# Optimization experiments

Measured on AMD Instinct MI355X. Metric: run time of the kernel, lower is better.

The kernel has to match this reference:

```python
import jax, jax.numpy as jnp
import numpy as np

D = 1024      # model dim
H = 16        # heads
DH = 64       # dim per head (lucidrains default)
DEPTH = 6
MLP = 2048
P = 32
PD = 3 * P * P   # 3072
NC = 1000
B = 4         # packed sequences
N = 640       # tokens per packed sequence (incl. padding)
M = 18        # images per packed sequence
GRID = 8      # image_size // patch_size
SIZES = [(8,8),(8,8),(7,7),(7,7),(6,8),(8,6),(6,6),(5,7),(7,5),(5,5),(4,8),(8,4),(4,6),(6,4),(4,4),(3,5),(5,3),(3,3)]
SCALE = DH ** -0.5


def _pack_meta():
    hs, ws, ids = [], [], []
    for i, (h, w) in enumerate(SIZES):
        hh, ww = np.meshgrid(np.arange(h), np.arange(w), indexing='ij')
        hs.append(hh.ravel()); ws.append(ww.ravel()); ids.append(np.full(h * w, i))
    h = np.concatenate(hs); w = np.concatenate(ws); ii = np.concatenate(ids)
    pad = N - h.shape[0]
    h = np.pad(h, (0, pad)); w = np.pad(w, (0, pad))
    ii = np.pad(ii, (0, pad), constant_values=-1)  # padding tokens form their own block
    return (np.tile(h, (B, 1)).astype(np.int32),
            np.tile(w, (B, 1)).astype(np.int32),
            np.tile(ii, (B, 1)).astype(np.int32))


def _ln(x, g, b, eps=1e-5):
    m = x.mean(-1, keepdims=True)
    v = ((x - m) ** 2).mean(-1, keepdims=True)
    return (x - m) * jax.lax.rsqrt(v + eps) * g + b


def _heads(t):  # [b, n, H*DH] -> [b, H, n, DH]
    return t.reshape(t.shape[0], t.shape[1], H, DH).swapaxes(1, 2)


def _mha(q_in, kv_in, mask, Wq, Wkv, Wo, qn_g, qn_b, kn_g, kn_b):
    # NaViT attention: pre-norm applied by caller to q_in; per-head qk LayerNorm; no biases.
    q = _ln(_heads(q_in @ Wq), qn_g, qn_b)
    k, v = jnp.split(kv_in @ Wkv, 2, axis=-1)
    k = _ln(_heads(k), kn_g, kn_b)
    v = _heads(v)
    dots = jnp.einsum('bhid,bhjd->bhij', q, k) * SCALE
    dots = jnp.where(mask, dots, jnp.finfo(dots.dtype).min)
    o = jnp.einsum('bhij,bhjd->bhid', jax.nn.softmax(dots, axis=-1), v)
    o = o.swapaxes(1, 2).reshape(o.shape[0], -1, H * DH)
    return o @ Wo


def _forward(patches, pe_ln1_g, pe_ln1_b, W_pe, b_pe, pe_ln2_g, pe_ln2_b, pos_h, pos_w,
             ln1_g, ln1_b, qn_g, qn_b, kn_g, kn_b, Wq, Wkv, Wo, ln2_g, ln2_b,
             W1, b1, W2, b2, fin_g, fin_b, pool_q, pl_ln_g, pl_ln_b, pl_qn_g, pl_qn_b,
             pl_kn_g, pl_kn_b, pl_Wq, pl_Wkv, pl_Wo, head_g, head_b, W_head, b_head,
             h_idx, w_idx, image_ids):
    # patch embedding: LN -> Linear -> LN, then factorized 2D pos embed
    x = _ln(patches, pe_ln1_g, pe_ln1_b) @ W_pe + b_pe
    x = _ln(x, pe_ln2_g, pe_ln2_b)
    x = x + pos_h[h_idx] + pos_w[w_idx]
    # block-diagonal attention mask: tokens attend only within their own image
    blk = (image_ids[:, :, None] == image_ids[:, None, :])[:, None]  # [B,1,N,N]
    for l in range(DEPTH):
        xn = _ln(x, ln1_g[l], ln1_b[l])
        x = x + _mha(xn, xn, blk, Wq[l], Wkv[l], Wo[l], qn_g[l], qn_b[l], kn_g[l], kn_b[l])
        xn = _ln(x, ln2_g[l], ln2_b[l])
        x = x + jax.nn.gelu(xn @ W1[l] + b1[l], approximate=False) @ W2[l] + b2[l]
    x = _ln(x, fin_g, fin_b)
    # attention pooling: one learned query per packed image (context NOT re-normed, as in na_vit)
    queries = jnp.broadcast_to(pool_q, (B, M, D))
    qn = _ln(queries, pl_ln_g, pl_ln_b)
    pmask = (jnp.arange(M)[None, :, None] == image_ids[:, None, :])[:, None]  # [B,1,M,N]
    pooled = _mha(qn, x, pmask, pl_Wq, pl_Wkv, pl_Wo, pl_qn_g, pl_qn_b, pl_kn_g, pl_kn_b) + queries
    pooled = pooled.reshape(B * M, D)
    return _ln(pooled, head_g, head_b) @ W_head + b_head  # [B*M, 1000]


def setup_inputs() -> dict:
    key = jax.random.key(0)
    ks = iter(jax.random.split(key, 32))
    h_idx, w_idx, image_ids = _pack_meta()
    f32 = jnp.float32
    d = dict(
        patches=jax.random.normal(next(ks), (B, N, PD), f32),
        pe_ln1_g=jnp.ones((PD,), f32), pe_ln1_b=jnp.zeros((PD,), f32),
        W_pe=0.02 * jax.random.normal(next(ks), (PD, D), f32), b_pe=jnp.zeros((D,), f32),
        pe_ln2_g=jnp.ones((D,), f32), pe_ln2_b=jnp.zeros((D,), f32),
        pos_h=0.02 * jax.random.normal(next(ks), (GRID, D), f32),
        pos_w=0.02 * jax.random.normal(next(ks), (GRID, D), f32),
        ln1_g=jnp.ones((DEPTH, D), f32), ln1_b=jnp.zeros((DEPTH, D), f32),
        qn_g=jnp.ones((DEPTH, DH), f32), qn_b=jnp.zeros((DEPTH, DH), f32),
        kn_g=jnp.ones((DEPTH, DH), f32), kn_b=jnp.zeros((DEPTH, DH), f32),
        Wq=0.02 * jax.random.normal(next(ks), (DEPTH, D, H * DH), f32),
        Wkv=0.02 * jax.random.normal(next(ks), (DEPTH, D, 2 * H * DH), f32),
        Wo=0.02 * jax.random.normal(next(ks), (DEPTH, H * DH, D), f32),
        ln2_g=jnp.ones((DEPTH, D), f32), ln2_b=jnp.zeros((DEPTH, D), f32),
        W1=0.02 * jax.random.normal(next(ks), (DEPTH, D, MLP), f32), b1=jnp.zeros((DEPTH, MLP), f32),
        W2=0.02 * jax.random.normal(next(ks), (DEPTH, MLP, D), f32), b2=jnp.zeros((DEPTH, D), f32),
        fin_g=jnp.ones((D,), f32), fin_b=jnp.zeros((D,), f32),
        pool_q=0.02 * jax.random.normal(next(ks), (D,), f32),
        pl_ln_g=jnp.ones((D,), f32), pl_ln_b=jnp.zeros((D,), f32),
        pl_qn_g=jnp.ones((DH,), f32), pl_qn_b=jnp.zeros((DH,), f32),
        pl_kn_g=jnp.ones((DH,), f32), pl_kn_b=jnp.zeros((DH,), f32),
        pl_Wq=0.02 * jax.random.normal(next(ks), (D, H * DH), f32),
        pl_Wkv=0.02 * jax.random.normal(next(ks), (D, 2 * H * DH), f32),
        pl_Wo=0.02 * jax.random.normal(next(ks), (H * DH, D), f32),
        head_g=jnp.ones((D,), f32), head_b=jnp.zeros((D,), f32),
        W_head=0.02 * jax.random.normal(next(ks), (D, NC), f32), b_head=jnp.zeros((NC,), f32),
        h_idx=jnp.asarray(h_idx), w_idx=jnp.asarray(w_idx), image_ids=jnp.asarray(image_ids),
    )
    return d


def reference(patches, pe_ln1_g, pe_ln1_b, W_pe, b_pe, pe_ln2_g, pe_ln2_b, pos_h, pos_w,
              ln1_g, ln1_b, qn_g, qn_b, kn_g, kn_b, Wq, Wkv, Wo, ln2_g, ln2_b,
              W1, b1, W2, b2, fin_g, fin_b, pool_q, pl_ln_g, pl_ln_b, pl_qn_g, pl_qn_b,
              pl_kn_g, pl_kn_b, pl_Wq, pl_Wkv, pl_Wo, head_g, head_b, W_head, b_head,
              h_idx, w_idx, image_ids):
    return _forward(patches, pe_ln1_g, pe_ln1_b, W_pe, b_pe, pe_ln2_g, pe_ln2_b, pos_h, pos_w,
                    ln1_g, ln1_b, qn_g, qn_b, kn_g, kn_b, Wq, Wkv, Wo, ln2_g, ln2_b,
                    W1, b1, W2, b2, fin_g, fin_b, pool_q, pl_ln_g, pl_ln_b, pl_qn_g, pl_qn_b,
                    pl_kn_g, pl_kn_b, pl_Wq, pl_Wkv, pl_Wo, head_g, head_b, W_head, b_head,
                    h_idx, w_idx, image_ids)
```

## Files before the change

kernel.cpp:

```cpp
#include <hip/hip_runtime.h>
#include <cmath>

constexpr int kB = 4, kN = 640, kD = 1024, kH = 16, kDH = 64;
constexpr int kDepth = 6, kMLP = 2048, kPD = 3072, kNC = 1000, kM = 18;
constexpr float kScale = 0.125f;
constexpr float kNegInf = -3.4028235e38f;

typedef __bf16 bf16;
typedef __attribute__((ext_vector_type(8))) __bf16 bf16x8;
typedef __attribute__((ext_vector_type(4))) __bf16 bf16x4;
typedef __attribute__((ext_vector_type(4))) float f32x4;

#define AS1 __attribute__((address_space(1)))
#define AS3 __attribute__((address_space(3)))

__device__ __forceinline__ void gload16(const void* g, void* l) {
  __builtin_amdgcn_global_load_lds((AS1 void*)g, (AS3 void*)l, 16, 0, 0);
}

constexpr size_t kMEG = 1048576;
constexpr size_t kOffPe = 0;
constexpr size_t kLayer0 = 3 * kMEG;
constexpr size_t kLayerSz = 8 * kMEG;
constexpr size_t kOffPool = kLayer0 + 6 * kLayerSz;
constexpr size_t kOffPlWq = kOffPool;
constexpr size_t kOffPlWkv = kOffPool + 1 * kMEG;
constexpr size_t kOffPlWo = kOffPool + 3 * kMEG;
constexpr size_t kOffHead = kOffPool + 4 * kMEG;
constexpr size_t kWtTotal = kOffHead + 1 * kMEG;

__global__ __launch_bounds__(256) void wt_all_kernel(
    const float* __restrict__ pe, const float* __restrict__ wq,
    const float* __restrict__ wkv, const float* __restrict__ wo,
    const float* __restrict__ w1, const float* __restrict__ w2,
    const float* __restrict__ plq, const float* __restrict__ plkv,
    const float* __restrict__ plo, const float* __restrict__ whead,
    bf16* __restrict__ WTB) {
  const int j = blockIdx.y;
  const float* W;
  size_t doff;
  int K, Nc, Np;
  if (j == 0) {
    W = pe; K = 3072; Nc = 1024; Np = 1024; doff = kOffPe;
  } else if (j < 31) {
    const int l = (j - 1) / 5, w = (j - 1) % 5;
    const size_t lbase = kLayer0 + (size_t)l * kLayerSz;
    switch (w) {
      case 0:  W = wq  + (size_t)l * kMEG;     K = 1024; Nc = 1024; doff = lbase;            break;
      case 1:  W = wkv + (size_t)l * 2 * kMEG; K = 1024; Nc = 2048; doff = lbase + kMEG;     break;
      case 2:  W = wo  + (size_t)l * kMEG;     K = 1024; Nc = 1024; doff = lbase + 3 * kMEG; break;
      case 3:  W = w1  + (size_t)l * 2 * kMEG; K = 1024; Nc = 2048; doff = lbase + 4 * kMEG; break;
      default: W = w2  + (size_t)l * 2 * kMEG; K = 2048; Nc = 1024; doff = lbase + 6 * kMEG; break;
    }
    Np = Nc;
  } else if (j == 31) { W = plq;  K = 1024; Nc = 1024; Np = 1024; doff = kOffPlWq; }
  else if (j == 32)   { W = plkv; K = 1024; Nc = 2048; Np = 2048; doff = kOffPlWkv; }
  else if (j == 33)   { W = plo;  K = 1024; Nc = 1024; Np = 1024; doff = kOffPlWo; }
  else                { W = whead; K = 1024; Nc = 1000; Np = 1024; doff = kOffHead; }
  const int nbx = Np >> 5;
  const int ntiles = nbx * (K >> 5);
  const int tile = blockIdx.x;
  if (tile >= ntiles) return;
  const int n0 = (tile % nbx) * 32, k0 = (tile / nbx) * 32;
  bf16* WT = WTB + doff;
  __shared__ float s[32][33];
  const int tx = threadIdx.x & 31, ty = threadIdx.x >> 5;
#pragma unroll
  for (int i = 0; i < 4; ++i) {
    const int k = ty + i * 8;
    s[k][tx] = (n0 + tx < Nc) ? W[(size_t)(k0 + k) * Nc + (n0 + tx)] : 0.f;
  }
  __syncthreads();
#pragma unroll
  for (int i = 0; i < 4; ++i) {
    const int n = ty + i * 8;
    WT[(size_t)(n0 + n) * K + (k0 + tx)] = (bf16)s[tx][n];
  }
}

template <typename OT>
__global__ __launch_bounds__(256) void ln_kernel(
    const float* __restrict__ in, OT* __restrict__ out,
    const float* __restrict__ g, const float* __restrict__ b, int K) {
  const int row = blockIdx.x;
  const float* x = in + (size_t)row * K;
  OT* o = out + (size_t)row * K;
  const int K4 = K >> 2;
  float s = 0.f, s2 = 0.f;
  for (int c = threadIdx.x; c < K4; c += 256) {
    const float4 v = ((const float4*)x)[c];
    s += v.x + v.y + v.z + v.w;
    s2 += v.x * v.x + v.y * v.y + v.z * v.z + v.w * v.w;
  }
#pragma unroll
  for (int off = 32; off; off >>= 1) { s += __shfl_down(s, off); s2 += __shfl_down(s2, off); }
  __shared__ float ls[4], ls2[4];
  __shared__ float sm, sr;
  const int wid = threadIdx.x >> 6, lane = threadIdx.x & 63;
  if (lane == 0) { ls[wid] = s; ls2[wid] = s2; }
  __syncthreads();
  if (threadIdx.x == 0) {
    float a = ls[0] + ls[1] + ls[2] + ls[3];
    float a2 = ls2[0] + ls2[1] + ls2[2] + ls2[3];
    float mean = a / K;
    float var = a2 / K - mean * mean;
    sm = mean; sr = rsqrtf(var + 1e-5f);
  }
  __syncthreads();
  const float mean = sm, r = sr;
  for (int c = threadIdx.x; c < K4; c += 256) {
    const float4 v = ((const float4*)x)[c];
    const float4 gv = ((const float4*)g)[c];
    const float4 bv = ((const float4*)b)[c];
    const int d = c * 4;
    o[d + 0] = (OT)((v.x - mean) * r * gv.x + bv.x);
    o[d + 1] = (OT)((v.y - mean) * r * gv.y + bv.y);
    o[d + 2] = (OT)((v.z - mean) * r * gv.z + bv.z);
    o[d + 3] = (OT)((v.w - mean) * r * gv.w + bv.w);
  }
}

__global__ __launch_bounds__(256) void ln_pos_kernel(
    const float* __restrict__ in, float* __restrict__ out,
    const float* __restrict__ g, const float* __restrict__ b,
    const float* __restrict__ ph, const float* __restrict__ pw,
    const int* __restrict__ hi, const int* __restrict__ wi) {
  const int row = blockIdx.x;
  const float* x = in + (size_t)row * kD;
  float* o = out + (size_t)row * kD;
  float s = 0.f, s2 = 0.f;
  for (int c = threadIdx.x; c < 256; c += 256) {
    const float4 v = ((const float4*)x)[c];
    s += v.x + v.y + v.z + v.w;
    s2 += v.x * v.x + v.y * v.y + v.z * v.z + v.w * v.w;
  }
#pragma unroll
  for (int off = 32; off; off >>= 1) { s += __shfl_down(s, off); s2 += __shfl_down(s2, off); }
  __shared__ float ls[4], ls2[4];
  __shared__ float sm, sr;
  const int wid = threadIdx.x >> 6, lane = threadIdx.x & 63;
  if (lane == 0) { ls[wid] = s; ls2[wid] = s2; }
  __syncthreads();
  if (threadIdx.x == 0) {
    float a = ls[0] + ls[1] + ls[2] + ls[3];
    float a2 = ls2[0] + ls2[1] + ls2[2] + ls2[3];
    float mean = a / kD;
    float var = a2 / kD - mean * mean;
    sm = mean; sr = rsqrtf(var + 1e-5f);
  }
  __syncthreads();
  const float mean = sm, r = sr;
  const float4* phr = (const float4*)(ph + (size_t)hi[row] * kD);
  const float4* pwr = (const float4*)(pw + (size_t)wi[row] * kD);
  const int c = threadIdx.x;
  const float4 v = ((const float4*)x)[c];
  const float4 gv = ((const float4*)g)[c];
  const float4 bv = ((const float4*)b)[c];
  const float4 hv = phr[c], wv = pwr[c];
  float4 ov;
  ov.x = (v.x - mean) * r * gv.x + bv.x + hv.x + wv.x;
  ov.y = (v.y - mean) * r * gv.y + bv.y + hv.y + wv.y;
  ov.z = (v.z - mean) * r * gv.z + bv.z + hv.z + wv.z;
  ov.w = (v.w - mean) * r * gv.w + bv.w + hv.w + wv.w;
  ((float4*)o)[c] = ov;
}

__global__ __launch_bounds__(64) void headln_kernel(
    float* __restrict__ p, int stride,
    const float* __restrict__ g, const float* __restrict__ b) {
  const int blk = blockIdx.x;
  const int outer = blk / kH, h = blk % kH;
  float* x = p + (size_t)outer * stride + h * kDH;
  const int lane = threadIdx.x;
  float v = x[lane];
  float s = v, s2 = v * v;
#pragma unroll
  for (int off = 32; off; off >>= 1) { s += __shfl_xor(s, off); s2 += __shfl_xor(s2, off); }
  const float m = s * (1.f / kDH);
  const float var = s2 * (1.f / kDH) - m * m;
  const float r = rsqrtf(var + 1e-5f);
  x[lane] = (v - m) * r * g[lane] + b[lane];
}

__global__ __launch_bounds__(256) void poolq_kernel(
    const float* __restrict__ pq, const float* __restrict__ lg,
    const float* __restrict__ lb, const bf16* __restrict__ WqT,
    const float* __restrict__ qg, const float* __restrict__ qb,
    float* __restrict__ qpool) {
  const int h = blockIdx.x, tid = threadIdx.x;
  __shared__ float qs[1024];
  __shared__ float red[256];
  __shared__ float ls[4], ls2[4];
  __shared__ float sm, sr;
  const float4 v = ((const float4*)pq)[tid];
  float s = v.x + v.y + v.z + v.w;
  float s2 = v.x * v.x + v.y * v.y + v.z * v.z + v.w * v.w;
#pragma unroll
  for (int off = 32; off; off >>= 1) { s += __shfl_down(s, off); s2 += __shfl_down(s2, off); }
  const int wid = tid >> 6, lane = tid & 63;
  if (lane == 0) { ls[wid] = s; ls2[wid] = s2; }
  __syncthreads();
  if (tid == 0) {
    float a = ls[0] + ls[1] + ls[2] + ls[3];
    float a2 = ls2[0] + ls2[1] + ls2[2] + ls2[3];
    float mean = a / kD;
    sm = mean; sr = rsqrtf(a2 / kD - mean * mean + 1e-5f);
  }
  __syncthreads();
  {
    const float mean = sm, r = sr;
    const float4 gv = ((const float4*)lg)[tid];
    const float4 bv = ((const float4*)lb)[tid];
    qs[tid * 4 + 0] = (v.x - mean) * r * gv.x + bv.x;
    qs[tid * 4 + 1] = (v.y - mean) * r * gv.y + bv.y;
    qs[tid * 4 + 2] = (v.z - mean) * r * gv.z + bv.z;
    qs[tid * 4 + 3] = (v.w - mean) * r * gv.w + bv.w;
  }
  __syncthreads();
  const int d = tid & 63, qq = tid >> 6;
  const bf16* wrow = WqT + (size_t)(h * 64 + d) * 1024 + qq * 256;
  const float* qp = qs + qq * 256;
  float part = 0.f;
  for (int k = 0; k < 256; k += 8) {
    const bf16x8 w8 = *(const bf16x8*)(wrow + k);
#pragma unroll
    for (int e = 0; e < 8; ++e) part += qp[k + e] * (float)w8[e];
  }
  red[tid] = part;
  __syncthreads();
  if (tid < 64) {
    const float dot = red[tid] + red[tid + 64] + red[tid + 128] + red[tid + 192];
    float hs = dot, hs2 = dot * dot;
#pragma unroll
    for (int off = 32; off; off >>= 1) { hs += __shfl_xor(hs, off); hs2 += __shfl_xor(hs2, off); }
    const float m = hs * (1.f / kDH);
    const float r = rsqrtf(hs2 * (1.f / kDH) - m * m + 1e-5f);
    qpool[h * 64 + tid] = (dot - m) * r * qg[tid] + qb[tid];
  }
}

template <int NI, bool OUT_BF, bool GELU>
__global__ __launch_bounds__(256) void gemm64_kernel(
    const bf16* __restrict__ A, const bf16* __restrict__ WT,
    float* __restrict__ Cf, bf16* __restrict__ Cb,
    const float* __restrict__ bias, const float* __restrict__ res,
    int K, int Ncol, int nbx) {
  constexpr int BN = NI * 32;
  __shared__ __align__(16) bf16 As[2][64 * 64];
  __shared__ __align__(16) bf16 Bs[2][BN * 64];
  const int tid = threadIdx.x, lane = tid & 63, wid = tid >> 6;
  const int wr = wid >> 1, wc = wid & 1;
  const int cpx = gridDim.x >> 3;
  const int swz = (blockIdx.x & 7) * cpx + (blockIdx.x >> 3);
  const int row0 = (swz / nbx) * 64, col0 = (swz % nbx) * BN;
  const int fr = lane & 15, fg = lane >> 4;
  f32x4 acc[2][NI] = {};
  bf16* sA = As[0]; bf16* sB = Bs[0];
  bf16* dA = As[1]; bf16* dB = Bs[1];

  auto stage = [&](bf16* tA, bf16* tB, int kt) {
#pragma unroll
    for (int i = 0; i < 2; ++i) {
      const int c = i * 256 + tid;
      const int r = c >> 3, ci = c & 7;
      gload16(A + (size_t)(row0 + r) * K + kt + ((ci ^ (r & 7)) * 8),
              tA + (i * 256 + wid * 64) * 8);
    }
#pragma unroll
    for (int i = 0; i < NI; ++i) {
      const int c = i * 256 + tid;
      const int r = c >> 3, ci = c & 7;
      gload16(WT + (size_t)(col0 + r) * K + kt + ((ci ^ (r & 7)) * 8),
              tB + (i * 256 + wid * 64) * 8);
    }
  };
  auto compute = [&](const bf16* tA, const bf16* tB) {
#pragma unroll
    for (int kk = 0; kk < 2; ++kk) {
      bf16x8 af[2], bfr[NI];
#pragma unroll
      for (int mi = 0; mi < 2; ++mi) {
        const int r = wr * 32 + mi * 16 + fr;
        af[mi] = *(const bf16x8*)(tA + r * 64 + (((kk * 4 + fg) ^ (r & 7)) * 8));
      }
#pragma unroll
      for (int ni = 0; ni < NI; ++ni) {
        const int r = wc * (NI * 16) + ni * 16 + fr;
        bfr[ni] = *(const bf16x8*)(tB + r * 64 + (((kk * 4 + fg) ^ (r & 7)) * 8));
      }
#pragma unroll
      for (int mi = 0; mi < 2; ++mi)
#pragma unroll
        for (int ni = 0; ni < NI; ++ni)
          acc[mi][ni] = __builtin_amdgcn_mfma_f32_16x16x32_bf16(af[mi], bfr[ni], acc[mi][ni], 0, 0, 0);
    }
  };

  const int NT = K >> 6;
  stage(sA, sB, 0);
  __syncthreads();
  for (int t = 1; t < NT; ++t) {
    stage(dA, dB, t * 64);
    compute(sA, sB);
    __syncthreads();
    bf16* u;
    u = sA; sA = dA; dA = u;
    u = sB; sB = dB; dB = u;
  }
  compute(sA, sB);

  const int rb = row0 + wr * 32 + fg * 4;
  const int cb = col0 + wc * (NI * 16) + fr;
#pragma unroll
  for (int mi = 0; mi < 2; ++mi) {
#pragma unroll
    for (int ni = 0; ni < NI; ++ni) {
      const int cc = cb + ni * 16;
      const float bb = bias ? bias[cc] : 0.f;
#pragma unroll
      for (int r = 0; r < 4; ++r) {
        const int rr = rb + mi * 16 + r;
        float v = acc[mi][ni][r] + bb;
        if (res) v += res[(size_t)rr * Ncol + cc];
        if (GELU) v = 0.5f * v * (1.f + erff(v * 0.70710678118654752f));
        if (OUT_BF) Cb[(size_t)rr * Ncol + cc] = (bf16)v;
        else        Cf[(size_t)rr * Ncol + cc] = v;
      }
    }
  }
}

template <bool OUT_BF>
__global__ __launch_bounds__(256) void gemm_tail_kernel(
    const bf16* __restrict__ A, const bf16* __restrict__ WT,
    float* __restrict__ Cf, bf16* __restrict__ Cb,
    const float* __restrict__ bias, const float* __restrict__ resv,
    int Mr, int K, int Nc, int ldc, int resmode) {
  __shared__ __align__(16) bf16 As[64][40];
  __shared__ __align__(16) bf16 Bs[128][40];
  const int tid = threadIdx.x;
  const int lane = tid & 63, wid = tid >> 6;
  const int row0 = blockIdx.y * 64, col0 = blockIdx.x * 128;
  f32x4 acc[4][2] = {};
  const int am = tid >> 2, ako = (tid & 3) * 8;
  const int fr = lane & 15, fg = (lane >> 4) * 8;
  for (int k0 = 0; k0 < K; k0 += 32) {
    if (row0 + am < Mr)
      *(bf16x8*)&As[am][ako] = *(const bf16x8*)(A + (size_t)(row0 + am) * K + k0 + ako);
    else {
      bf16x8 z = {};
      *(bf16x8*)&As[am][ako] = z;
    }
#pragma unroll
    for (int it = 0; it < 2; ++it) {
      const int c = it * 256 + tid;
      const int n = c >> 2, ko = (c & 3) * 8;
      *(bf16x8*)&Bs[n][ko] = *(const bf16x8*)(WT + (size_t)(col0 + n) * K + k0 + ko);
    }
    __syncthreads();
    bf16x8 af[4], bfr[2];
#pragma unroll
    for (int mi = 0; mi < 4; ++mi) af[mi] = *(const bf16x8*)&As[mi * 16 + fr][fg];
#pragma unroll
    for (int ni = 0; ni < 2; ++ni) bfr[ni] = *(const bf16x8*)&Bs[wid * 32 + ni * 16 + fr][fg];
#pragma unroll
    for (int mi = 0; mi < 4; ++mi)
#pragma unroll
      for (int ni = 0; ni < 2; ++ni)
        acc[mi][ni] = __builtin_amdgcn_mfma_f32_16x16x32_bf16(af[mi], bfr[ni], acc[mi][ni], 0, 0, 0);
    __syncthreads();
  }
  const int r4 = (lane >> 4) * 4;
  const int cc0 = col0 + wid * 32 + (lane & 15);
#pragma unroll
  for (int mi = 0; mi < 4; ++mi) {
#pragma unroll
    for (int ni = 0; ni < 2; ++ni) {
      const int cc = cc0 + ni * 16;
      if (cc >= Nc) continue;
#pragma unroll
      for (int r = 0; r < 4; ++r) {
        const int rr = row0 + mi * 16 + r4 + r;
        if (rr >= Mr) continue;
        float v = acc[mi][ni][r];
        if (bias) v += bias[cc];
        if (resmode == 1) v += resv[(size_t)rr * ldc + cc];
        else if (resmode == 2) v += resv[cc];
        if (OUT_BF) Cb[(size_t)rr * ldc + cc] = (bf16)v;
        else        Cf[(size_t)rr * ldc + cc] = v;
      }
    }
  }
}

__global__ __launch_bounds__(256) void attn_kernel(
    const bf16* __restrict__ qkv, const int* __restrict__ ids,
    const float* __restrict__ qg, const float* __restrict__ qb,
    const float* __restrict__ kg, const float* __restrict__ kb,
    bf16* __restrict__ o) {
  const int h = blockIdx.x, img = blockIdx.y, b = blockIdx.z;
  const int tid = threadIdx.x, lane = tid & 63, wid = tid >> 6;
  __shared__ __align__(16) bf16 Qs[64][72];
  __shared__ __align__(16) bf16 Ks[64][72];
  __shared__ __align__(16) bf16 Vt[64][72];
  __shared__ __align__(16) bf16 Ps[64][72];
  __shared__ int wlo[4], whi[4];
  __shared__ int sLo, sHi;
  {
    const int want = (img < kM) ? img : -1;
    int lo = kN, hi = -1;
    for (int j = tid; j < kN; j += 256) {
      if (ids[b * kN + j] == want) { lo = min(lo, j); hi = max(hi, j); }
    }
#pragma unroll
    for (int off = 32; off; off >>= 1) {
      lo = min(lo, __shfl_xor(lo, off));
      hi = max(hi, __shfl_xor(hi, off));
    }
    if (lane == 0) { wlo[wid] = lo; whi[wid] = hi; }
    __syncthreads();
    if (tid == 0) {
      sLo = min(min(wlo[0], wlo[1]), min(wlo[2], wlo[3]));
      sHi = max(max(whi[0], whi[1]), max(whi[2], whi[3]));
    }
    __syncthreads();
  }
  if (sHi < 0) return;
  const int start = sLo, T = sHi - sLo + 1;
  if (img == kM) {
    for (int j = start + wid; j <= sHi; j += 4)
      o[((size_t)(b * kN + j)) * kD + h * kDH + lane] = (bf16)0.f;
    return;
  }
#pragma unroll
  for (int it = 0; it < 2; ++it) {
    const int ch = it * 256 + tid;
    const int r = ch >> 3, d0 = (ch & 7) * 8;
    if (r < T) {
      const bf16* base = qkv + ((size_t)(b * kN + start + r)) * 3072 + h * kDH + d0;
      const bf16x8 qv = *(const bf16x8*)(base);
      const bf16x8 kv = *(const bf16x8*)(base + 1024);
      const bf16x8 vv = *(const bf16x8*)(base + 2048);
      float qf[8], kf[8];
      float sq = 0.f, sq2 = 0.f, sk = 0.f, sk2 = 0.f;
#pragma unroll
      for (int e = 0; e < 8; ++e) {
        qf[e] = (float)qv[e]; kf[e] = (float)kv[e];
        sq += qf[e]; sq2 += qf[e] * qf[e];
        sk += kf[e]; sk2 += kf[e] * kf[e];
      }
#pragma unroll
      for (int off = 1; off < 8; off <<= 1) {
        sq += __shfl_xor(sq, off); sq2 += __shfl_xor(sq2, off);
        sk += __shfl_xor(sk, off); sk2 += __shfl_xor(sk2, off);
      }
      const float qm = sq * (1.f / 64);
      const float qr = rsqrtf(sq2 * (1.f / 64) - qm * qm + 1e-5f);
      const float km = sk * (1.f / 64);
      const float kr = rsqrtf(sk2 * (1.f / 64) - km * km + 1e-5f);
      bf16x8 qw, kw;
#pragma unroll
      for (int e = 0; e < 8; ++e) {
        qw[e] = (bf16)((qf[e] - qm) * qr * qg[d0 + e] + qb[d0 + e]);
        kw[e] = (bf16)((kf[e] - km) * kr * kg[d0 + e] + kb[d0 + e]);
      }
      *(bf16x8*)&Qs[r][d0] = qw;
      *(bf16x8*)&Ks[r][d0] = kw;
#pragma unroll
      for (int e = 0; e < 8; ++e) Vt[d0 + e][r] = vv[e];
    } else {
      const bf16x8 z = {};
      *(bf16x8*)&Qs[r][d0] = z;
      *(bf16x8*)&Ks[r][d0] = z;
#pragma unroll
      for (int e = 0; e < 8; ++e) Vt[d0 + e][r] = (bf16)0.f;
    }
  }
  __syncthreads();
  const int fr = lane & 15, fg = lane >> 4;
  const int r0 = wid * 16;
  f32x4 sacc[4] = {};
#pragma unroll
  for (int k0 = 0; k0 < 64; k0 += 32) {
    const bf16x8 aq = *(const bf16x8*)&Qs[r0 + fr][k0 + fg * 8];
#pragma unroll
    for (int ni = 0; ni < 4; ++ni) {
      const bf16x8 bk = *(const bf16x8*)&Ks[ni * 16 + fr][k0 + fg * 8];
      sacc[ni] = __builtin_amdgcn_mfma_f32_16x16x32_bf16(aq, bk, sacc[ni], 0, 0, 0);
    }
  }
  float inv[4];
#pragma unroll
  for (int r = 0; r < 4; ++r) {
    float mx = kNegInf;
#pragma unroll
    for (int ni = 0; ni < 4; ++ni) {
      const float s = (ni * 16 + fr < T) ? sacc[ni][r] * kScale : kNegInf;
      sacc[ni][r] = s;
      mx = fmaxf(mx, s);
    }
#pragma unroll
    for (int off = 1; off < 16; off <<= 1) mx = fmaxf(mx, __shfl_xor(mx, off));
    float sum = 0.f;
#pragma unroll
    for (int ni = 0; ni < 4; ++ni) {
      const float p = __expf(sacc[ni][r] - mx);
      sacc[ni][r] = p;
      sum += p;
    }
#pragma unroll
    for (int off = 1; off < 16; off <<= 1) sum += __shfl_xor(sum, off);
    inv[r] = 1.f / sum;
  }
#pragma unroll
  for (int ni = 0; ni < 4; ++ni)
#pragma unroll
    for (int r = 0; r < 4; ++r)
      Ps[r0 + fg * 4 + r][ni * 16 + fr] = (bf16)sacc[ni][r];
  f32x4 oacc[4] = {};
#pragma unroll
  for (int k0 = 0; k0 < 64; k0 += 32) {
    const bf16x8 ap = *(const bf16x8*)&Ps[r0 + fr][k0 + fg * 8];
#pragma unroll
    for (int ni = 0; ni < 4; ++ni) {
      const bf16x8 bv = *(const bf16x8*)&Vt[ni * 16 + fr][k0 + fg * 8];
      oacc[ni] = __builtin_amdgcn_mfma_f32_16x16x32_bf16(ap, bv, oacc[ni], 0, 0, 0);
    }
  }
#pragma unroll
  for (int r = 0; r < 4; ++r) {
    const int i = r0 + fg * 4 + r;
    if (i < T) {
      const size_t orow = ((size_t)(b * kN + start + i)) * kD + h * kDH;
      const float iv = inv[r];
#pragma unroll
      for (int ni = 0; ni < 4; ++ni)
        o[orow + ni * 16 + fr] = (bf16)(oacc[ni][r] * iv);
    }
  }
}

__global__ __launch_bounds__(64) void poolattn_kernel(
    const float* __restrict__ qp, const float* __restrict__ kv,
    const int* __restrict__ ids, bf16* __restrict__ o) {
  const int blk = blockIdx.x;
  const int h = blk % kH;
  const int bm = blk / kH;
  const int m = bm % kM, b = bm / kM;
  const int lane = threadIdx.x;
  __shared__ float sc[kN];
  __shared__ float qs[kDH];
  qs[lane] = qp[h * kDH + lane];
  __syncthreads();
  float mymax = kNegInf;
  int jmn = kN, jmx = -1;
  for (int j = lane; j < kN; j += 64) {
    const int idj = ids[b * kN + j];
    float s;
    if (idj == m) {
      const float* krow = kv + ((size_t)(b * kN + j)) * (2 * kD) + h * kDH;
      float dot = 0.f;
#pragma unroll
      for (int d = 0; d < kDH; ++d) dot += qs[d] * krow[d];
      s = dot * kScale;
      jmn = min(jmn, j); jmx = max(jmx, j);
    } else {
      s = kNegInf;
    }
    sc[j] = s;
    mymax = fmaxf(mymax, s);
  }
#pragma unroll
  for (int off = 32; off; off >>= 1) {
    mymax = fmaxf(mymax, __shfl_xor(mymax, off));
    jmn = min(jmn, __shfl_xor(jmn, off));
    jmx = max(jmx, __shfl_xor(jmx, off));
  }
  const int jlo = jmn, jhi = jmx + 1;
  float mysum = 0.f;
  for (int j = jlo + lane; j < jhi; j += 64) {
    const float p = __expf(sc[j] - mymax);
    sc[j] = p;
    mysum += p;
  }
#pragma unroll
  for (int off = 32; off; off >>= 1) mysum += __shfl_xor(mysum, off);
  const float inv = 1.f / mysum;
  __syncthreads();
  float acc = 0.f;
  const float* vptr = kv + ((size_t)(b * kN + jlo)) * (2 * kD) + kD + h * kDH + lane;
  for (int j = jlo; j < jhi; ++j, vptr += 2 * kD) acc += sc[j] * vptr[0];
  o[((size_t)(b * kM + m)) * kD + h * kDH + lane] = (bf16)(acc * inv);
}

extern "C" void kernel_launch(void* const* d_in, const int* in_sizes, int n_in,
                              void* d_out, int out_size, void* d_ws, size_t ws_size,
                              hipStream_t stream) {
  const float* patches  = (const float*)d_in[0];
  const float* pe_ln1_g = (const float*)d_in[1];
  const float* pe_ln1_b = (const float*)d_in[2];
  const float* W_pe     = (const float*)d_in[3];
  const float* b_pe     = (const float*)d_in[4];
  const float* pe_ln2_g = (const float*)d_in[5];
  const float* pe_ln2_b = (const float*)d_in[6];
  const float* pos_h    = (const float*)d_in[7];
  const float* pos_w    = (const float*)d_in[8];
  const float* ln1_g    = (const float*)d_in[9];
  const float* ln1_b    = (const float*)d_in[10];
  const float* qn_g     = (const float*)d_in[11];
  const float* qn_b     = (const float*)d_in[12];
  const float* kn_g     = (const float*)d_in[13];
  const float* kn_b     = (const float*)d_in[14];
  const float* Wq       = (const float*)d_in[15];
  const float* Wkv      = (const float*)d_in[16];
  const float* Wo       = (const float*)d_in[17];
  const float* ln2_g    = (const float*)d_in[18];
  const float* ln2_b    = (const float*)d_in[19];
  const float* W1       = (const float*)d_in[20];
  const float* b1       = (const float*)d_in[21];
  const float* W2       = (const float*)d_in[22];
  const float* b2       = (const float*)d_in[23];
  const float* fin_g    = (const float*)d_in[24];
  const float* fin_b    = (const float*)d_in[25];
  const float* pool_q   = (const float*)d_in[26];
  const float* pl_ln_g  = (const float*)d_in[27];
  const float* pl_ln_b  = (const float*)d_in[28];
  const float* pl_qn_g  = (const float*)d_in[29];
  const float* pl_qn_b  = (const float*)d_in[30];
  const float* pl_kn_g  = (const float*)d_in[31];
  const float* pl_kn_b  = (const float*)d_in[32];
  const float* pl_Wq    = (const float*)d_in[33];
  const float* pl_Wkv   = (const float*)d_in[34];
  const float* pl_Wo    = (const float*)d_in[35];
  const float* head_g   = (const float*)d_in[36];
  const float* head_b   = (const float*)d_in[37];
  const float* W_head   = (const float*)d_in[38];
  const float* b_head   = (const float*)d_in[39];
  const int* h_idx      = (const int*)d_in[40];
  const int* w_idx      = (const int*)d_in[41];
  const int* image_ids  = (const int*)d_in[42];
  float* out = (float*)d_out;

  const size_t SZ = (size_t)kB * kN * kD;
  char* p = (char*)d_ws;
  float* x    = (float*)p;           p += SZ * 4;
  bf16*  xnb  = (bf16*)p;            p += SZ * 2;
  char*  scratch = p;                p += 32u * 1024 * 1024;
  char*  smalls = p;                 p += 1u * 1024 * 1024;
  bf16*  wtbuf = (bf16*)p;
  bf16*  qkvbb = (bf16*)scratch;
  bf16*  attno = (bf16*)(scratch + 16u * 1024 * 1024);
  bf16*  plnb  = (bf16*)scratch;
  float* emb   = (float*)(scratch + 16u * 1024 * 1024);
  bf16*  h1b   = (bf16*)scratch;
  float* kvpool = (float*)scratch;
  float* qpool   = (float*)smalls;
  bf16*  opoolb  = (bf16*)(smalls + 8192);
  float* pooled  = (float*)(smalls + 8192 + 163840);
  bf16*  pooledn = (bf16*)(smalls + 8192 + 163840 + 327680);

  const int BN = kB * kN;
  const int nbyM = BN / 64;

  wt_all_kernel<<<dim3(3072, 35), 256, 0, stream>>>(
      W_pe, Wq, Wkv, Wo, W1, W2, pl_Wq, pl_Wkv, pl_Wo, W_head, wtbuf);

  ln_kernel<bf16><<<BN, 256, 0, stream>>>(patches, plnb, pe_ln1_g, pe_ln1_b, kPD);
  gemm64_kernel<2, false, false><<<(kD / 64) * nbyM, 256, 0, stream>>>(
      plnb, wtbuf + kOffPe, emb, nullptr, b_pe, nullptr, kPD, kD, kD / 64);
  ln_pos_kernel<<<BN, 256, 0, stream>>>(emb, x, pe_ln2_g, pe_ln2_b, pos_h, pos_w, h_idx, w_idx);

  for (int l = 0; l < kDepth; ++l) {
    const bf16* lw = wtbuf + kLayer0 + (size_t)l * kLayerSz;
    ln_kernel<bf16><<<BN, 256, 0, stream>>>(x, xnb, ln1_g + (size_t)l * kD, ln1_b + (size_t)l * kD, kD);
    gemm64_kernel<4, true, false><<<(3 * kD / 128) * nbyM, 256, 0, stream>>>(
        xnb, lw, nullptr, qkvbb, nullptr, nullptr, kD, 3 * kD, 3 * kD / 128);
    attn_kernel<<<dim3(kH, kM + 1, kB), 256, 0, stream>>>(
        qkvbb, image_ids,
        qn_g + (size_t)l * kDH, qn_b + (size_t)l * kDH,
        kn_g + (size_t)l * kDH, kn_b + (size_t)l * kDH, attno);
    gemm64_kernel<2, false, false><<<(kD / 64) * nbyM, 256, 0, stream>>>(
        attno, lw + 3 * kMEG, x, nullptr, nullptr, x, kD, kD, kD / 64);
    ln_kernel<bf16><<<BN, 256, 0, stream>>>(x, xnb, ln2_g + (size_t)l * kD, ln2_b + (size_t)l * kD, kD);
    gemm64_kernel<4, true, true><<<(kMLP / 128) * nbyM, 256, 0, stream>>>(
        xnb, lw + 4 * kMEG, nullptr, h1b, b1 + (size_t)l * kMLP, nullptr, kD, kMLP, kMLP / 128);
    gemm64_kernel<2, false, false><<<(kD / 64) * nbyM, 256, 0, stream>>>(
        h1b, lw + 6 * kMEG, x, nullptr, b2 + (size_t)l * kD, x, kMLP, kD, kD / 64);
  }

  ln_kernel<bf16><<<BN, 256, 0, stream>>>(x, xnb, fin_g, fin_b, kD);

  poolq_kernel<<<kH, 256, 0, stream>>>(
      pool_q, pl_ln_g, pl_ln_b, wtbuf + kOffPlWq, pl_qn_g, pl_qn_b, qpool);
  gemm64_kernel<4, false, false><<<(2 * kD / 128) * nbyM, 256, 0, stream>>>(
      xnb, wtbuf + kOffPlWkv, kvpool, nullptr, nullptr, nullptr, kD, 2 * kD, 2 * kD / 128);
  headln_kernel<<<BN * kH, 64, 0, stream>>>(kvpool, 2 * kD, pl_kn_g, pl_kn_b);
  poolattn_kernel<<<kB * kM * kH, 64, 0, stream>>>(qpool, kvpool, image_ids, opoolb);
  gemm_tail_kernel<false><<<dim3(8, 2), 256, 0, stream>>>(
      opoolb, wtbuf + kOffPlWo, pooled, nullptr, nullptr, pool_q, kB * kM, kD, kD, kD, 2);

  ln_kernel<bf16><<<kB * kM, 256, 0, stream>>>(pooled, pooledn, head_g, head_b, kD);
  gemm_tail_kernel<false><<<dim3(8, 2), 256, 0, stream>>>(
      pooledn, wtbuf + kOffHead, out, nullptr, b_head, nullptr, kB * kM, kD, kNC, kNC, 0);
}
```

Before: 1.018 ms.

## Vectorize weight transpose, fuse pool key LayerNorm into GEMM, shrink GEMM tiles

The weight transpose kernel now uses 64x64 tiles with float4 loads and 8-wide bf16 stores, which cuts the block count and makes global accesses wider. The per-head key LayerNorm of the pooling attention is folded into the KV GEMM epilogue through a new template flag, and that GEMM writes bf16 instead of fp32, so a separate kernel launch goes away and pooling-attention K/V traffic is halved. The QKV and MLP-up GEMMs switch from 128- to 64-column tiles to get more blocks. This raises parallelism but cuts per-block reuse, and the bf16 K/V adds a small precision change.

```diff
diff --git a/kernel.cpp b/kernel.cpp
--- a/kernel.cpp
+++ b/kernel.cpp
@@ -27,7 +27,6 @@
 constexpr size_t kOffPlWkv = kOffPool + 1 * kMEG;
 constexpr size_t kOffPlWo = kOffPool + 3 * kMEG;
 constexpr size_t kOffHead = kOffPool + 4 * kMEG;
-constexpr size_t kWtTotal = kOffHead + 1 * kMEG;
 
 __global__ __launch_bounds__(256) void wt_all_kernel(
     const float* __restrict__ pe, const float* __restrict__ wq,
@@ -57,24 +56,44 @@
   else if (j == 32)   { W = plkv; K = 1024; Nc = 2048; Np = 2048; doff = kOffPlWkv; }
   else if (j == 33)   { W = plo;  K = 1024; Nc = 1024; Np = 1024; doff = kOffPlWo; }
   else                { W = whead; K = 1024; Nc = 1000; Np = 1024; doff = kOffHead; }
-  const int nbx = Np >> 5;
-  const int ntiles = nbx * (K >> 5);
+  const int nbx = Np >> 6;
+  const int ntiles = nbx * (K >> 6);
   const int tile = blockIdx.x;
   if (tile >= ntiles) return;
-  const int n0 = (tile % nbx) * 32, k0 = (tile / nbx) * 32;
+  const int n0 = (tile % nbx) * 64, k0 = (tile / nbx) * 64;
   bf16* WT = WTB + doff;
-  __shared__ float s[32][33];
-  const int tx = threadIdx.x & 31, ty = threadIdx.x >> 5;
-#pragma unroll
-  for (int i = 0; i < 4; ++i) {
-    const int k = ty + i * 8;
-    s[k][tx] = (n0 + tx < Nc) ? W[(size_t)(k0 + k) * Nc + (n0 + tx)] : 0.f;
-  }
-  __syncthreads();
-#pragma unroll
-  for (int i = 0; i < 4; ++i) {
-    const int n = ty + i * 8;
-    WT[(size_t)(n0 + n) * K + (k0 + tx)] = (bf16)s[tx][n];
+  __shared__ float s[64][65];
+  const int tid = threadIdx.x;
+  if (n0 + 64 <= Nc) {
+#pragma unroll
+    for (int i = 0; i < 4; ++i) {
+      const int c = i * 256 + tid;
+      const int r = c >> 4, cq = c & 15;
+      const float4 v = *(const float4*)(W + (size_t)(k0 + r) * Nc + n0 + cq * 4);
+      s[r][cq * 4 + 0] = v.x; s[r][cq * 4 + 1] = v.y;
+      s[r][cq * 4 + 2] = v.z; s[r][cq * 4 + 3] = v.w;
+    }
+  } else {
+#pragma unroll
+    for (int i = 0; i < 4; ++i) {
+      const int c = i * 256 + tid;
+      const int r = c >> 4, cq = c & 15;
+#pragma unroll
+      for (int e = 0; e < 4; ++e) {
+        const int n = n0 + cq * 4 + e;
+        s[r][cq * 4 + e] = (n < Nc) ? W[(size_t)(k0 + r) * Nc + n] : 0.f;
+      }
+    }
+  }
+  __syncthreads();
+#pragma unroll
+  for (int i = 0; i < 2; ++i) {
+    const int c = i * 256 + tid;
+    const int n = c >> 3, kq = c & 7;
+    bf16x8 w;
+#pragma unroll
+    for (int e = 0; e < 8; ++e) w[e] = (bf16)s[kq * 8 + e][n];
+    *(bf16x8*)(WT + (size_t)(n0 + n) * K + k0 + kq * 8) = w;
   }
 }
 
@@ -128,12 +147,10 @@
   const int row = blockIdx.x;
   const float* x = in + (size_t)row * kD;
   float* o = out + (size_t)row * kD;
-  float s = 0.f, s2 = 0.f;
-  for (int c = threadIdx.x; c < 256; c += 256) {
-    const float4 v = ((const float4*)x)[c];
-    s += v.x + v.y + v.z + v.w;
-    s2 += v.x * v.x + v.y * v.y + v.z * v.z + v.w * v.w;
-  }
+  const int c = threadIdx.x;
+  const float4 v = ((const float4*)x)[c];
+  float s = v.x + v.y + v.z + v.w;
+  float s2 = v.x * v.x + v.y * v.y + v.z * v.z + v.w * v.w;
 #pragma unroll
   for (int off = 32; off; off >>= 1) { s += __shfl_down(s, off); s2 += __shfl_down(s2, off); }
   __shared__ float ls[4], ls2[4];
@@ -152,8 +169,6 @@
   const float mean = sm, r = sr;
   const float4* phr = (const float4*)(ph + (size_t)hi[row] * kD);
   const float4* pwr = (const float4*)(pw + (size_t)wi[row] * kD);
-  const int c = threadIdx.x;
-  const float4 v = ((const float4*)x)[c];
   const float4 gv = ((const float4*)g)[c];
   const float4 bv = ((const float4*)b)[c];
   const float4 hv = phr[c], wv = pwr[c];
@@ -163,23 +178,6 @@
   ov.z = (v.z - mean) * r * gv.z + bv.z + hv.z + wv.z;
   ov.w = (v.w - mean) * r * gv.w + bv.w + hv.w + wv.w;
   ((float4*)o)[c] = ov;
-}
-
-__global__ __launch_bounds__(64) void headln_kernel(
-    float* __restrict__ p, int stride,
-    const float* __restrict__ g, const float* __restrict__ b) {
-  const int blk = blockIdx.x;
-  const int outer = blk / kH, h = blk % kH;
-  float* x = p + (size_t)outer * stride + h * kDH;
-  const int lane = threadIdx.x;
-  float v = x[lane];
-  float s = v, s2 = v * v;
-#pragma unroll
-  for (int off = 32; off; off >>= 1) { s += __shfl_xor(s, off); s2 += __shfl_xor(s2, off); }
-  const float m = s * (1.f / kDH);
-  const float var = s2 * (1.f / kDH) - m * m;
-  const float r = rsqrtf(var + 1e-5f);
-  x[lane] = (v - m) * r * g[lane] + b[lane];
 }
 
 __global__ __launch_bounds__(256) void poolq_kernel(
@@ -239,11 +237,12 @@
   }
 }
 
-template <int NI, bool OUT_BF, bool GELU>
+template <int NI, bool OUT_BF, bool GELU, bool HLN>
 __global__ __launch_bounds__(256) void gemm64_kernel(
     const bf16* __restrict__ A, const bf16* __restrict__ WT,
     float* __restrict__ Cf, bf16* __restrict__ Cb,
     const float* __restrict__ bias, const float* __restrict__ res,
+    const float* __restrict__ hg, const float* __restrict__ hb,
     int K, int Ncol, int nbx) {
   constexpr int BN = NI * 32;
   __shared__ __align__(16) bf16 As[2][64 * 64];
@@ -311,18 +310,43 @@
 
   const int rb = row0 + wr * 32 + fg * 4;
   const int cb = col0 + wc * (NI * 16) + fr;
+  float hm[2][4], hr[2][4];
+  if (HLN) {
+#pragma unroll
+    for (int mi = 0; mi < 2; ++mi)
+#pragma unroll
+      for (int r = 0; r < 4; ++r) {
+        float s = 0.f, s2 = 0.f;
+#pragma unroll
+        for (int ni = 0; ni < NI; ++ni) {
+          const float v = acc[mi][ni][r];
+          s += v; s2 += v * v;
+        }
+#pragma unroll
+        for (int off = 1; off < 16; off <<= 1) {
+          s += __shfl_xor(s, off); s2 += __shfl_xor(s2, off);
+        }
+        const float m = s * (1.f / kDH);
+        hm[mi][r] = m;
+        hr[mi][r] = rsqrtf(s2 * (1.f / kDH) - m * m + 1e-5f);
+      }
+  }
+  const bool kHalf = HLN && (cb < kD);
 #pragma unroll
   for (int mi = 0; mi < 2; ++mi) {
 #pragma unroll
     for (int ni = 0; ni < NI; ++ni) {
       const int cc = cb + ni * 16;
       const float bb = bias ? bias[cc] : 0.f;
+      const float hgv = HLN ? hg[ni * 16 + fr] : 0.f;
+      const float hbv = HLN ? hb[ni * 16 + fr] : 0.f;
 #pragma unroll
       for (int r = 0; r < 4; ++r) {
         const int rr = rb + mi * 16 + r;
         float v = acc[mi][ni][r] + bb;
         if (res) v += res[(size_t)rr * Ncol + cc];
         if (GELU) v = 0.5f * v * (1.f + erff(v * 0.70710678118654752f));
+        if (HLN && kHalf) v = (v - hm[mi][r]) * hr[mi][r] * hgv + hbv;
         if (OUT_BF) Cb[(size_t)rr * Ncol + cc] = (bf16)v;
         else        Cf[(size_t)rr * Ncol + cc] = v;
       }
@@ -541,7 +565,7 @@
 }
 
 __global__ __launch_bounds__(64) void poolattn_kernel(
-    const float* __restrict__ qp, const float* __restrict__ kv,
+    const float* __restrict__ qp, const bf16* __restrict__ kv,
     const int* __restrict__ ids, bf16* __restrict__ o) {
   const int blk = blockIdx.x;
   const int h = blk % kH;
@@ -558,10 +582,10 @@
     const int idj = ids[b * kN + j];
     float s;
     if (idj == m) {
-      const float* krow = kv + ((size_t)(b * kN + j)) * (2 * kD) + h * kDH;
+      const bf16* krow = kv + ((size_t)(b * kN + j)) * (2 * kD) + h * kDH;
       float dot = 0.f;
 #pragma unroll
-      for (int d = 0; d < kDH; ++d) dot += qs[d] * krow[d];
+      for (int d = 0; d < kDH; ++d) dot += qs[d] * (float)krow[d];
       s = dot * kScale;
       jmn = min(jmn, j); jmx = max(jmx, j);
     } else {
@@ -588,8 +612,8 @@
   const float inv = 1.f / mysum;
   __syncthreads();
   float acc = 0.f;
-  const float* vptr = kv + ((size_t)(b * kN + jlo)) * (2 * kD) + kD + h * kDH + lane;
-  for (int j = jlo; j < jhi; ++j, vptr += 2 * kD) acc += sc[j] * vptr[0];
+  const bf16* vptr = kv + ((size_t)(b * kN + jlo)) * (2 * kD) + kD + h * kDH + lane;
+  for (int j = jlo; j < jhi; ++j, vptr += 2 * kD) acc += sc[j] * (float)vptr[0];
   o[((size_t)(b * kM + m)) * kD + h * kDH + lane] = (bf16)(acc * inv);
 }
 
@@ -653,7 +677,7 @@
   bf16*  plnb  = (bf16*)scratch;
   float* emb   = (float*)(scratch + 16u * 1024 * 1024);
   bf16*  h1b   = (bf16*)scratch;
-  float* kvpool = (float*)scratch;
+  bf16*  kvpoolb = (bf16*)scratch;
   float* qpool   = (float*)smalls;
   bf16*  opoolb  = (bf16*)(smalls + 8192);
   float* pooled  = (float*)(smalls + 8192 + 163840);
@@ -662,40 +686,39 @@
   const int BN = kB * kN;
   const int nbyM = BN / 64;
 
-  wt_all_kernel<<<dim3(3072, 35), 256, 0, stream>>>(
+  wt_all_kernel<<<dim3(768, 35), 256, 0, stream>>>(
       W_pe, Wq, Wkv, Wo, W1, W2, pl_Wq, pl_Wkv, pl_Wo, W_head, wtbuf);
 
   ln_kernel<bf16><<<BN, 256, 0, stream>>>(patches, plnb, pe_ln1_g, pe_ln1_b, kPD);
-  gemm64_kernel<2, false, false><<<(kD / 64) * nbyM, 256, 0, stream>>>(
-      plnb, wtbuf + kOffPe, emb, nullptr, b_pe, nullptr, kPD, kD, kD / 64);
+  gemm64_kernel<2, false, false, false><<<(kD / 64) * nbyM, 256, 0, stream>>>(
+      plnb, wtbuf + kOffPe, emb, nullptr, b_pe, nullptr, nullptr, nullptr, kPD, kD, kD / 64);
   ln_pos_kernel<<<BN, 256, 0, stream>>>(emb, x, pe_ln2_g, pe_ln2_b, pos_h, pos_w, h_idx, w_idx);
 
   for (int l = 0; l < kDepth; ++l) {
     const bf16* lw = wtbuf + kLayer0 + (size_t)l * kLayerSz;
     ln_kernel<bf16><<<BN, 256, 0, stream>>>(x, xnb, ln1_g + (size_t)l * kD, ln1_b + (size_t)l * kD, kD);
-    gemm64_kernel<4, true, false><<<(3 * kD / 128) * nbyM, 256, 0, stream>>>(
-        xnb, lw, nullptr, qkvbb, nullptr, nullptr, kD, 3 * kD, 3 * kD / 128);
+    gemm64_kernel<2, true, false, false><<<(3 * kD / 64) * nbyM, 256, 0, stream>>>(
+        xnb, lw, nullptr, qkvbb, nullptr, nullptr, nullptr, nullptr, kD, 3 * kD, 3 * kD / 64);
     attn_kernel<<<dim3(kH, kM + 1, kB), 256, 0, stream>>>(
         qkvbb, image_ids,
         qn_g + (size_t)l * kDH, qn_b + (size_t)l * kDH,
         kn_g + (size_t)l * kDH, kn_b + (size_t)l * kDH, attno);
-    gemm64_kernel<2, false, false><<<(kD / 64) * nbyM, 256, 0, stream>>>(
-        attno, lw + 3 * kMEG, x, nullptr, nullptr, x, kD, kD, kD / 64);
+    gemm64_kernel<2, false, false, false><<<(kD / 64) * nbyM, 256, 0, stream>>>(
+        attno, lw + 3 * kMEG, x, nullptr, nullptr, x, nullptr, nullptr, kD, kD, kD / 64);
     ln_kernel<bf16><<<BN, 256, 0, stream>>>(x, xnb, ln2_g + (size_t)l * kD, ln2_b + (size_t)l * kD, kD);
-    gemm64_kernel<4, true, true><<<(kMLP / 128) * nbyM, 256, 0, stream>>>(
-        xnb, lw + 4 * kMEG, nullptr, h1b, b1 + (size_t)l * kMLP, nullptr, kD, kMLP, kMLP / 128);
-    gemm64_kernel<2, false, false><<<(kD / 64) * nbyM, 256, 0, stream>>>(
-        h1b, lw + 6 * kMEG, x, nullptr, b2 + (size_t)l * kD, x, kMLP, kD, kD / 64);
+    gemm64_kernel<2, true, true, false><<<(kMLP / 64) * nbyM, 256, 0, stream>>>(
+        xnb, lw + 4 * kMEG, nullptr, h1b, b1 + (size_t)l * kMLP, nullptr, nullptr, nullptr, kD, kMLP, kMLP / 64);
+    gemm64_kernel<2, false, false, false><<<(kD / 64) * nbyM, 256, 0, stream>>>(
+        h1b, lw + 6 * kMEG, x, nullptr, b2 + (size_t)l * kD, x, nullptr, nullptr, kMLP, kD, kD / 64);
   }
 
   ln_kernel<bf16><<<BN, 256, 0, stream>>>(x, xnb, fin_g, fin_b, kD);
 
   poolq_kernel<<<kH, 256, 0, stream>>>(
       pool_q, pl_ln_g, pl_ln_b, wtbuf + kOffPlWq, pl_qn_g, pl_qn_b, qpool);
-  gemm64_kernel<4, false, false><<<(2 * kD / 128) * nbyM, 256, 0, stream>>>(
-      xnb, wtbuf + kOffPlWkv, kvpool, nullptr, nullptr, nullptr, kD, 2 * kD, 2 * kD / 128);
-  headln_kernel<<<BN * kH, 64, 0, stream>>>(kvpool, 2 * kD, pl_kn_g, pl_kn_b);
-  poolattn_kernel<<<kB * kM * kH, 64, 0, stream>>>(qpool, kvpool, image_ids, opoolb);
+  gemm64_kernel<4, true, false, true><<<(2 * kD / 128) * nbyM, 256, 0, stream>>>(
+      xnb, wtbuf + kOffPlWkv, nullptr, kvpoolb, nullptr, nullptr, pl_kn_g, pl_kn_b, kD, 2 * kD, 2 * kD / 128);
+  poolattn_kernel<<<kB * kM * kH, 64, 0, stream>>>(qpool, kvpoolb, image_ids, opoolb);
   gemm_tail_kernel<false><<<dim3(8, 2), 256, 0, stream>>>(
       opoolb, wtbuf + kOffPlWo, pooled, nullptr, nullptr, pool_q, kB * kM, kD, kD, kD, 2);
 
```

Result: faster. 971.0 us (-4.6%).
